# Kernel optimization log

Hardware: AMD Instinct MI355X
Metric: run time of the kernel (lower is better)

## Reference

```python
import jax, jax.numpy as jnp
import numpy as np

NUM_TAGS = 96
PAD_IDX = 0
NEG = -10000.0


def setup_inputs() -> dict:
    key = jax.random.key(0)
    k1, k2, k3, k4, k5 = jax.random.split(key, 5)
    B, S, T = 128, 2048, NUM_TAGS
    emissions = jax.random.normal(k1, (B, S, T), dtype=jnp.float32)
    tags = jax.random.randint(k2, (B, S), 0, T, dtype=jnp.int64)
    mask = jnp.ones((B, S), dtype=jnp.float32)
    transitions = jax.random.normal(k3, (T, T), dtype=jnp.float32)
    transitions = transitions.at[PAD_IDX, :].set(NEG)
    transitions = transitions.at[:, PAD_IDX].set(NEG)
    transitions = transitions.at[PAD_IDX, PAD_IDX].set(0.0)
    start_transitions = jax.random.normal(k4, (T,), dtype=jnp.float32)
    start_transitions = start_transitions.at[PAD_IDX].set(NEG)
    end_transitions = jax.random.normal(k5, (T,), dtype=jnp.float32)
    return {"emissions": emissions, "tags": tags, "mask": mask,
            "transitions": transitions, "start_transitions": start_transitions,
            "end_transitions": end_transitions}


def _compute_score(emissions, tags, mask, transitions, start_transitions, end_transitions):
    # score of the gold path, fully vectorized over time
    score = start_transitions[tags[:, 0]]
    score = score + jnp.take_along_axis(emissions[:, 0], tags[:, 0:1], axis=1)[:, 0]
    trans = transitions[tags[:, :-1], tags[:, 1:]]                       # (B, S-1)
    emit = jnp.take_along_axis(emissions[:, 1:], tags[:, 1:, None], axis=2)[..., 0]
    score = score + jnp.sum((trans + emit) * mask[:, 1:], axis=1)
    last_pos = mask.astype(jnp.int32).sum(axis=1) - 1                    # (B,)
    last_tags = jnp.take_along_axis(tags, last_pos[:, None], axis=1)[:, 0]
    return score + end_transitions[last_tags]


def _log_partition(emissions, mask, transitions, start_transitions, end_transitions):
    # forward algorithm as a scan over time, alpha kept resident
    alpha0 = start_transitions[None, :] + emissions[:, 0]                # (B, T)
    em_rest = jnp.swapaxes(emissions[:, 1:], 0, 1)                       # (S-1, B, T)
    mk_rest = jnp.swapaxes(mask[:, 1:], 0, 1)                            # (S-1, B)

    def step(alpha, xs):
        emit_t, m_t = xs
        # (B, T_prev, T_next)
        nxt = jax.nn.logsumexp(alpha[:, :, None] + transitions[None] + emit_t[:, None, :], axis=1)
        m = m_t[:, None]
        return nxt * m + alpha * (1.0 - m), None

    alpha, _ = jax.lax.scan(step, alpha0, (em_rest, mk_rest))
    return jax.nn.logsumexp(alpha + end_transitions[None, :], axis=1)


def reference(emissions, tags, mask, transitions, start_transitions, end_transitions):
    mask = mask.astype(jnp.float32)
    log_num = _compute_score(emissions, tags, mask, transitions, start_transitions, end_transitions)
    log_den = _log_partition(emissions, mask, transitions, start_transitions, end_transitions)
    return jnp.mean(log_den - log_num)
```

## Files before the change

### kernel.cpp

```cpp
#include <hip/hip_runtime.h>
#include <hip/hip_bf16.h>
#include <math.h>

#define NTAG 96
#define NB   128
#define SLEN 2048
#define CPERB (SLEN * NTAG)
#define NCH  16
#define CHUNK 128

typedef __attribute__((ext_vector_type(8)))  short bf16x8;
typedef __attribute__((ext_vector_type(4)))  float f32x4;
typedef __attribute__((ext_vector_type(16))) float f32x16;
union U8 { unsigned int u[4]; bf16x8 v; };

__device__ __forceinline__ unsigned int pk2bf(float lo, float hi) {
    union { __hip_bfloat16 h; unsigned short u; } a, b;
    a.h = __float2bfloat16(lo);
    b.h = __float2bfloat16(hi);
    return (unsigned int)a.u | ((unsigned int)b.u << 16);
}
__device__ __forceinline__ float bf16lo(unsigned int u) {
    union { unsigned int i; float f; } x; x.i = u << 16; return x.f;
}
__device__ __forceinline__ float bf16hi(unsigned int u) {
    union { unsigned int i; float f; } x; x.i = u & 0xffff0000u; return x.f;
}

__device__ __forceinline__ float waveSum(float v) {
    #pragma unroll
    for (int o = 32; o > 0; o >>= 1) v += __shfl_xor(v, o);
    return v;
}

__global__ __launch_bounds__(256) void exp_pass_bf16(
    const float* __restrict__ x, unsigned int* __restrict__ y)
{
    size_t i = (size_t)blockIdx.x * 256 + threadIdx.x;
    f32x4 v = ((const f32x4*)x)[i];
    uint2 o;
    o.x = pk2bf(__expf(v[0]), __expf(v[1]));
    o.y = pk2bf(__expf(v[2]), __expf(v[3]));
    ((uint2*)y)[i] = o;
}

template <int IEXP>
__global__ __launch_bounds__(64, 2) void crf_chunk32(
    const void* __restrict__ srcE, const float* __restrict__ mask,
    const float* __restrict__ trans,
    float* __restrict__ P, float* __restrict__ Pls)
{
    const int tid = threadIdx.x;
    const int c = tid & 31;
    const int h = tid >> 5;

    const int k   = blockIdx.x;
    const int xcd = k & 7;
    const int seq = k >> 3;
    const int w2  = seq % 3;
    const int bcg = seq / 3;
    const int bc  = bcg * 8 + xcd;
    const int cch = bc & (NCH - 1);
    const int b   = bc >> 4;
    const int t0  = 1 + cch * CHUNK;
    const int t1  = min(SLEN, t0 + CHUNK);

    float tm = -1e30f;
    for (int q = tid; q < NTAG * NTAG; q += 64) tm = fmaxf(tm, trans[q]);
    #pragma unroll
    for (int o = 32; o > 0; o >>= 1) tm = fmaxf(tm, __shfl_xor(tm, o));
    const float tmax = tm;

    const int cS = (c & 0x13) | ((c & 4) << 1) | ((c & 8) >> 1);
    U8 Af[3][6];
    #pragma unroll
    for (int jt = 0; jt < 3; ++jt) {
        #pragma unroll
        for (int kt = 0; kt < 6; ++kt) {
            #pragma unroll
            for (int d = 0; d < 4; ++d) {
                int K0 = 16 * kt + 8 * (d >> 1) + 4 * h + 2 * (d & 1);
                int J  = 32 * jt + cS;
                Af[jt][kt].u[d] = pk2bf(
                    __expf(trans[K0 * NTAG + J] - tmax),
                    __expf(trans[(K0 + 1) * NTAG + J] - tmax));
            }
        }
    }

    float S[3][16];
    #pragma unroll
    for (int rt = 0; rt < 3; ++rt) {
        #pragma unroll
        for (int r = 0; r < 16; ++r)
            S[rt][r] = (32 * rt + (r & 3) + 8 * (r >> 2) + 4 * h == 32 * w2 + c)
                       ? 1.0f : 0.0f;
    }
    float ls = 0.0f;

#define RENORM() do { \
    float mx_ = S[0][0]; \
    _Pragma("unroll") \
    for (int rt_ = 0; rt_ < 3; ++rt_) { \
        _Pragma("unroll") \
        for (int r_ = 0; r_ < 16; ++r_) mx_ = fmaxf(mx_, S[rt_][r_]); \
    } \
    mx_ = fmaxf(mx_, __shfl_xor(mx_, 32)); \
    mx_ = fmaxf(mx_, 1e-30f); \
    float inv_ = 1.0f / mx_; \
    ls += __logf(mx_); \
    _Pragma("unroll") \
    for (int rt_ = 0; rt_ < 3; ++rt_) { \
        _Pragma("unroll") \
        for (int r_ = 0; r_ < 16; ++r_) S[rt_][r_] *= inv_; \
    } \
} while (0)

    U8 Bu[6];
#define MAKEB() do { \
    _Pragma("unroll") \
    for (int kt_ = 0; kt_ < 6; ++kt_) { \
        const int rt_ = kt_ >> 1; \
        _Pragma("unroll") \
        for (int d_ = 0; d_ < 4; ++d_) { \
            const int rb_ = 8 * (kt_ & 1) + 4 * (d_ >> 1) + 2 * (d_ & 1); \
            Bu[kt_].u[d_] = pk2bf(S[rt_][rb_], S[rt_][rb_ + 1]); \
        } \
    } \
} while (0)

    const float* mkB = mask + (size_t)b * SLEN;
    const f32x16 z16 = {0.f,0.f,0.f,0.f,0.f,0.f,0.f,0.f,
                        0.f,0.f,0.f,0.f,0.f,0.f,0.f,0.f};

    const unsigned short* eH = (const unsigned short*)srcE + (size_t)b * CPERB;
    const float*          eF = (const float*)srcE + (size_t)b * CPERB;

    uint2 E2[12];
    f32x4 E4[12];
#define LOADE(T) do { \
    if (IEXP) { \
        const float* pE_ = eF + (size_t)(T) * NTAG + 4 * h; \
        _Pragma("unroll") \
        for (int rt_ = 0; rt_ < 3; ++rt_) { \
            _Pragma("unroll") \
            for (int q_ = 0; q_ < 4; ++q_) \
                E4[rt_ * 4 + q_] = *(const f32x4*)(pE_ + 32 * rt_ + 8 * q_); \
        } \
    } else { \
        const unsigned short* pH_ = eH + (size_t)(T) * NTAG + 4 * h; \
        _Pragma("unroll") \
        for (int rt_ = 0; rt_ < 3; ++rt_) { \
            _Pragma("unroll") \
            for (int q_ = 0; q_ < 4; ++q_) \
                E2[rt_ * 4 + q_] = *(const uint2*)(pH_ + 32 * rt_ + 8 * q_); \
        } \
    } \
} while (0)

#define STEPCORE(T) do { \
    LOADE(T); \
    f32x16 a0, a1, a2; \
    a0 = __builtin_amdgcn_mfma_f32_32x32x16_bf16(Af[0][0].v, Bu[0].v, z16, 0, 0, 0); \
    a1 = __builtin_amdgcn_mfma_f32_32x32x16_bf16(Af[1][0].v, Bu[0].v, z16, 0, 0, 0); \
    a2 = __builtin_amdgcn_mfma_f32_32x32x16_bf16(Af[2][0].v, Bu[0].v, z16, 0, 0, 0); \
    _Pragma("unroll") \
    for (int kt_ = 1; kt_ < 6; ++kt_) { \
        a0 = __builtin_amdgcn_mfma_f32_32x32x16_bf16(Af[0][kt_].v, Bu[kt_].v, a0, 0, 0, 0); \
        a1 = __builtin_amdgcn_mfma_f32_32x32x16_bf16(Af[1][kt_].v, Bu[kt_].v, a1, 0, 0, 0); \
        a2 = __builtin_amdgcn_mfma_f32_32x32x16_bf16(Af[2][kt_].v, Bu[kt_].v, a2, 0, 0, 0); \
    } \
    float mv_ = mkB[(T)]; \
    if (mv_ != 0.0f) { \
        _Pragma("unroll") \
        for (int rt_ = 0; rt_ < 3; ++rt_) { \
            f32x16 ac_ = (rt_ == 0) ? a0 : ((rt_ == 1) ? a1 : a2); \
            _Pragma("unroll") \
            for (int q_ = 0; q_ < 4; ++q_) { \
                float e0_, e1_, e2_, e3_; \
                if (IEXP) { \
                    e0_ = __expf(E4[rt_ * 4 + q_][0]); \
                    e1_ = __expf(E4[rt_ * 4 + q_][1]); \
                    e2_ = __expf(E4[rt_ * 4 + q_][2]); \
                    e3_ = __expf(E4[rt_ * 4 + q_][3]); \
                } else { \
                    uint2 u_ = E2[rt_ * 4 + q_]; \
                    e0_ = bf16lo(u_.x); e1_ = bf16hi(u_.x); \
                    e2_ = bf16lo(u_.y); e3_ = bf16hi(u_.y); \
                } \
                S[rt_][4 * q_ + 0] = ac_[4 * q_ + 0] * e0_; \
                S[rt_][4 * q_ + 1] = ac_[4 * q_ + 1] * e1_; \
                S[rt_][4 * q_ + 2] = ac_[4 * q_ + 2] * e2_; \
                S[rt_][4 * q_ + 3] = ac_[4 * q_ + 3] * e3_; \
            } \
        } \
        ls += tmax; \
    } \
} while (0)

#define STEP(T)   do { STEPCORE(T); MAKEB(); } while (0)
#define STEP_R(T) do { STEPCORE(T); RENORM(); MAKEB(); } while (0)

    MAKEB();

    const int nsteps = t1 - t0;
    const int nfull  = nsteps >> 3;
    int t = t0;
    #pragma unroll 1
    for (int blk = 0; blk < nfull; ++blk, t += 8) {
        STEP(t + 0); STEP(t + 1); STEP(t + 2); STEP(t + 3);
        STEP(t + 4); STEP(t + 5); STEP(t + 6); STEP_R(t + 7);
    }
    #pragma unroll 1
    while (t < t1) { STEP_R(t); ++t; }

    float* Pb = P + ((size_t)bc * NTAG + (32 * w2 + c)) * NTAG + 4 * h;
    #pragma unroll
    for (int rt = 0; rt < 3; ++rt) {
        #pragma unroll
        for (int q = 0; q < 4; ++q) {
            f32x4 v;
            v[0] = S[rt][4 * q + 0]; v[1] = S[rt][4 * q + 1];
            v[2] = S[rt][4 * q + 2]; v[3] = S[rt][4 * q + 3];
            *(f32x4*)(Pb + 32 * rt + 8 * q) = v;
        }
    }
    if (h == 0) Pls[(size_t)bc * NTAG + 32 * w2 + c] = ls;
#undef STEP
#undef STEP_R
#undef STEPCORE
#undef LOADE
#undef MAKEB
#undef RENORM
}

__global__ __launch_bounds__(128) void crf_fold(
    const float* __restrict__ em, const float* __restrict__ startT,
    const float* __restrict__ endT,
    const float* __restrict__ P, const float* __restrict__ Pls,
    float* __restrict__ den)
{
    __shared__ float aS[NTAG];
    __shared__ float sRed[2];
    const int b = blockIdx.x, tid = threadIdx.x;
    const bool act = tid < NTAG;

    float A = act ? (startT[tid] + em[(size_t)b * CPERB + tid]) : -1e30f;

    for (int c = 0; c < NCH; ++c) {
        const size_t bc = (size_t)b * NCH + c;
        float v = act ? (A + Pls[bc * NTAG + tid]) : -1e30f;
        float mv = v;
        #pragma unroll
        for (int o = 32; o > 0; o >>= 1) mv = fmaxf(mv, __shfl_xor(mv, o));
        if ((tid & 63) == 0) sRed[tid >> 6] = mv;
        __syncthreads();
        const float m = fmaxf(sRed[0], sRed[1]);
        __syncthreads();
        if (act) aS[tid] = __expf(v - m);
        __syncthreads();
        if (act) {
            const float* Pc = P + bc * (NTAG * NTAG) + tid;
            float dot = 0.f;
            #pragma unroll 8
            for (int i = 0; i < NTAG; ++i)
                dot = fmaf(aS[i], Pc[(size_t)i * NTAG], dot);
            A = m + __logf(dot);
        }
        __syncthreads();
    }

    float Afin = act ? (A + endT[tid]) : -1e30f;
    float mv = Afin;
    #pragma unroll
    for (int o = 32; o > 0; o >>= 1) mv = fmaxf(mv, __shfl_xor(mv, o));
    if ((tid & 63) == 0) sRed[tid >> 6] = mv;
    __syncthreads();
    const float m2 = fmaxf(sRed[0], sRed[1]);
    __syncthreads();
    float ex = act ? __expf(Afin - m2) : 0.f;
    ex = waveSum(ex);
    if ((tid & 63) == 0) sRed[tid >> 6] = ex;
    __syncthreads();
    if (tid == 0) den[b] = m2 + __logf(sRed[0] + sRed[1]);
}

__global__ __launch_bounds__(64, 1) void crf_forward_seq(
    const float* __restrict__ srcE, const float* __restrict__ srcM,
    const float* __restrict__ trans, const float* __restrict__ startT,
    const float* __restrict__ endT, float* __restrict__ den)
{
    __shared__ unsigned int lbuf[2][48 * 20];
    const int tid = threadIdx.x;
    const int g = tid >> 4;
    const int b16 = tid & 15;
    const int b = blockIdx.x * 16 + b16;

    float tm = -1e30f;
    for (int q = tid; q < NTAG * NTAG; q += 64) tm = fmaxf(tm, trans[q]);
    #pragma unroll
    for (int o = 32; o > 0; o >>= 1) tm = fmaxf(tm, __shfl_xor(tm, o));
    const float tmax = tm;

    bf16x8 Af[6][3];
    #pragma unroll
    for (int jt = 0; jt < 6; ++jt) {
        #pragma unroll
        for (int kf = 0; kf < 3; ++kf) {
            U8 u;
            #pragma unroll
            for (int d = 0; d < 4; ++d) {
                int i0 = 32 * kf + 8 * g + 2 * d;
                int j = 16 * jt + b16;
                u.u[d] = pk2bf(__expf(trans[i0 * NTAG + j] - tmax),
                               __expf(trans[(i0 + 1) * NTAG + j] - tmax));
            }
            Af[jt][kf] = u.v;
        }
    }

    float al[24];
    #pragma unroll
    for (int tile = 0; tile < 6; ++tile) {
        #pragma unroll
        for (int r = 0; r < 4; ++r) {
            int j = 16 * tile + 4 * g + r;
            al[tile * 4 + r] = __expf(startT[j]) * __expf(srcE[(size_t)b * CPERB + j]);
        }
    }
    float ls = 0.0f;

#define RENORM2() do { \
    float mx_ = al[0]; \
    _Pragma("unroll") \
    for (int k_ = 1; k_ < 24; ++k_) mx_ = fmaxf(mx_, al[k_]); \
    mx_ = fmaxf(mx_, __shfl_xor(mx_, 16)); \
    mx_ = fmaxf(mx_, __shfl_xor(mx_, 32)); \
    mx_ = fmaxf(mx_, 1e-30f); \
    float inv_ = 1.0f / mx_; \
    ls += __logf(mx_); \
    _Pragma("unroll") \
    for (int k_ = 0; k_ < 24; ++k_) al[k_] *= inv_; \
} while (0)

    U8 Bu[3];
#define MAKEB2(BUF) do { \
    _Pragma("unroll") \
    for (int t_ = 0; t_ < 6; ++t_) { \
        lbuf[BUF][(8 * t_ + 2 * g) * 20 + b16]     = pk2bf(al[4 * t_ + 0], al[4 * t_ + 1]); \
        lbuf[BUF][(8 * t_ + 2 * g + 1) * 20 + b16] = pk2bf(al[4 * t_ + 2], al[4 * t_ + 3]); \
    } \
    __syncthreads(); \
    _Pragma("unroll") \
    for (int kf_ = 0; kf_ < 3; ++kf_) { \
        _Pragma("unroll") \
        for (int d_ = 0; d_ < 4; ++d_) \
            Bu[kf_].u[d_] = lbuf[BUF][(16 * kf_ + 4 * g + d_) * 20 + b16]; \
    } \
} while (0)

    RENORM2();
    MAKEB2(0);
    const f32x4 zf4 = {0.f, 0.f, 0.f, 0.f};

    #pragma unroll 1
    for (int t = 1; t < SLEN; ++t) {
        f32x4 E[6];
        #pragma unroll
        for (int tl = 0; tl < 6; ++tl)
            E[tl] = *(const f32x4*)(srcE + (size_t)b * CPERB + (size_t)t * NTAG + 16 * tl + 4 * g);
        float mv = srcM[(size_t)b * SLEN + t];
        f32x4 acc[6];
        #pragma unroll
        for (int jt = 0; jt < 6; ++jt) {
            f32x4 a_ = __builtin_amdgcn_mfma_f32_16x16x32_bf16(Af[jt][0], Bu[0].v, zf4, 0, 0, 0);
            a_ = __builtin_amdgcn_mfma_f32_16x16x32_bf16(Af[jt][1], Bu[1].v, a_, 0, 0, 0);
            a_ = __builtin_amdgcn_mfma_f32_16x16x32_bf16(Af[jt][2], Bu[2].v, a_, 0, 0, 0);
            acc[jt] = a_;
        }
        bool km = (mv != 0.0f);
        #pragma unroll
        for (int tile = 0; tile < 6; ++tile) {
            #pragma unroll
            for (int r = 0; r < 4; ++r) {
                float nv = acc[tile][r] * __expf(E[tile][r]);
                al[tile * 4 + r] = km ? nv : al[tile * 4 + r];
            }
        }
        ls += km ? tmax : 0.0f;
        if ((t & 3) == 0) RENORM2();
        MAKEB2(t & 1);
        __syncthreads();
    }

    float s = 0.f;
    #pragma unroll
    for (int tile = 0; tile < 6; ++tile) {
        #pragma unroll
        for (int r = 0; r < 4; ++r) {
            int j = 16 * tile + 4 * g + r;
            s += al[tile * 4 + r] * __expf(endT[j]);
        }
    }
    s += __shfl_xor(s, 16);
    s += __shfl_xor(s, 32);
    if (tid < 16) den[b] = ls + __logf(s);
#undef MAKEB2
#undef RENORM2
}

__global__ __launch_bounds__(256) void crf_score(
    const float* __restrict__ em, const int* __restrict__ tags,
    const float* __restrict__ mask, const float* __restrict__ trans,
    const float* __restrict__ startT, const float* __restrict__ endT,
    float* __restrict__ num)
{
    __shared__ float sS[4], sM[4];
    const int b = blockIdx.x, tid = threadIdx.x;
    const float* emB = em + (size_t)b * CPERB;
    const int* tgB = tags + (size_t)b * SLEN;
    const float* mkB = mask + (size_t)b * SLEN;

    float part = 0.f, mcnt = 0.f;
    for (int t = tid; t < SLEN; t += 256) {
        float mt = mkB[t];
        mcnt += mt;
        if (t >= 1) {
            int tp = tgB[t - 1], tc = tgB[t];
            part += (trans[tp * NTAG + tc] + emB[(size_t)t * NTAG + tc]) * mt;
        }
    }
    part = waveSum(part);
    mcnt = waveSum(mcnt);
    if ((tid & 63) == 0) { sS[tid >> 6] = part; sM[tid >> 6] = mcnt; }
    __syncthreads();
    if (tid == 0) {
        float tot = sS[0] + sS[1] + sS[2] + sS[3];
        int last = (int)(sM[0] + sM[1] + sM[2] + sM[3]) - 1;
        int t0 = tgB[0];
        num[b] = tot + startT[t0] + emB[t0] + endT[tgB[last]];
    }
}

__global__ __launch_bounds__(128) void crf_final(
    const float* __restrict__ den, const float* __restrict__ num,
    float* __restrict__ out)
{
    __shared__ float s2[2];
    const int tid = threadIdx.x;
    float v = den[tid] - num[tid];
    v = waveSum(v);
    if ((tid & 63) == 0) s2[tid >> 6] = v;
    __syncthreads();
    if (tid == 0) out[0] = (s2[0] + s2[1]) * (1.0f / NB);
}

extern "C" void kernel_launch(void* const* d_in, const int* in_sizes, int n_in,
                              void* d_out, int out_size, void* d_ws, size_t ws_size,
                              hipStream_t stream) {
    const float* em     = (const float*)d_in[0];
    const int*   tags   = (const int*)d_in[1];
    const float* mask   = (const float*)d_in[2];
    const float* trans  = (const float*)d_in[3];
    const float* startT = (const float*)d_in[4];
    const float* endT   = (const float*)d_in[5];
    float* out = (float*)d_out;
    float* num = (float*)d_ws;
    float* den = num + NB;

    const size_t szP   = (size_t)NB * NCH * NTAG * NTAG;
    const size_t szPls = (size_t)NB * NCH * NTAG;
    float* P    = (float*)((char*)d_ws + 4096);
    float* Pls  = P + szP;
    unsigned int* eexpH = (unsigned int*)(Pls + szPls);
    const size_t need_mid  = 4096 + (szP + szPls) * 4;
    const size_t need_full = need_mid + (size_t)NB * CPERB * 2;

    crf_score<<<NB, 256, 0, stream>>>(em, tags, mask, trans, startT, endT, num);
    if (ws_size >= need_full) {
        exp_pass_bf16<<<(NB * CPERB) / (256 * 4), 256, 0, stream>>>(em, eexpH);
        crf_chunk32<0><<<3 * NB * NCH, 64, 0, stream>>>(eexpH, mask, trans, P, Pls);
        crf_fold<<<NB, 128, 0, stream>>>(em, startT, endT, P, Pls, den);
    } else if (ws_size >= need_mid) {
        crf_chunk32<1><<<3 * NB * NCH, 64, 0, stream>>>(em, mask, trans, P, Pls);
        crf_fold<<<NB, 128, 0, stream>>>(em, startT, endT, P, Pls, den);
    } else {
        crf_forward_seq<<<NB / 16, 64, 0, stream>>>(em, mask, trans, startT, endT, den);
    }
    crf_final<<<1, 128, 0, stream>>>(den, num, out);
}
```

Before: 710.4 us.

## Double-buffer emission loads and pack four chunk waves per block

Emission loads for step t+1 are now issued before the MFMA chain of step t, using two register buffers that alternate between steps. This hides global-load latency behind the matrix ops of the sequential chunk scan. Each block also becomes 4 waves (256 threads) instead of 1, with the grid divided by 4, which changes occupancy and scheduling. The remainder loop is unrolled into guarded steps so the buffer parity stays fixed, and the extra buffers raise register pressure.

```diff
diff --git a/kernel.cpp b/kernel.cpp
--- a/kernel.cpp
+++ b/kernel.cpp
@@ -45,18 +45,20 @@
 }
 
 template <int IEXP>
-__global__ __launch_bounds__(64, 2) void crf_chunk32(
+__global__ __launch_bounds__(256, 2) void crf_chunk32(
     const void* __restrict__ srcE, const float* __restrict__ mask,
     const float* __restrict__ trans,
     float* __restrict__ P, float* __restrict__ Pls)
 {
-    const int tid = threadIdx.x;
-    const int c = tid & 31;
-    const int h = tid >> 5;
-
-    const int k   = blockIdx.x;
-    const int xcd = k & 7;
-    const int seq = k >> 3;
+    const int wv  = threadIdx.x >> 6;
+    const int ln  = threadIdx.x & 63;
+    const int c = ln & 31;
+    const int h = ln >> 5;
+
+    const int blk = blockIdx.x;
+    const int xcd = blk & 7;
+    const int grp = blk >> 3;
+    const int seq = grp * 4 + wv;
     const int w2  = seq % 3;
     const int bcg = seq / 3;
     const int bc  = bcg * 8 + xcd;
@@ -66,7 +68,7 @@
     const int t1  = min(SLEN, t0 + CHUNK);
 
     float tm = -1e30f;
-    for (int q = tid; q < NTAG * NTAG; q += 64) tm = fmaxf(tm, trans[q]);
+    for (int q = ln; q < NTAG * NTAG; q += 64) tm = fmaxf(tm, trans[q]);
     #pragma unroll
     for (int o = 32; o > 0; o >>= 1) tm = fmaxf(tm, __shfl_xor(tm, o));
     const float tmax = tm;
@@ -133,33 +135,34 @@
     const f32x16 z16 = {0.f,0.f,0.f,0.f,0.f,0.f,0.f,0.f,
                         0.f,0.f,0.f,0.f,0.f,0.f,0.f,0.f};
 
-    const unsigned short* eH = (const unsigned short*)srcE + (size_t)b * CPERB;
-    const float*          eF = (const float*)srcE + (size_t)b * CPERB;
-
-    uint2 E2[12];
-    f32x4 E4[12];
-#define LOADE(T) do { \
+    const unsigned short* eHp = (const unsigned short*)srcE + (size_t)b * CPERB;
+    const float*          eFp = (const float*)srcE + (size_t)b * CPERB;
+
+    uint2 EH0[12], EH1[12];
+    f32x4 EF0[12], EF1[12];
+#define LOADE(N, T) do { \
+    int tn_ = (T) < t1 ? (T) : (t1 - 1); \
     if (IEXP) { \
-        const float* pE_ = eF + (size_t)(T) * NTAG + 4 * h; \
+        const float* pE_ = eFp + (size_t)tn_ * NTAG + 4 * h; \
         _Pragma("unroll") \
         for (int rt_ = 0; rt_ < 3; ++rt_) { \
             _Pragma("unroll") \
             for (int q_ = 0; q_ < 4; ++q_) \
-                E4[rt_ * 4 + q_] = *(const f32x4*)(pE_ + 32 * rt_ + 8 * q_); \
+                EF##N[rt_ * 4 + q_] = *(const f32x4*)(pE_ + 32 * rt_ + 8 * q_); \
         } \
     } else { \
-        const unsigned short* pH_ = eH + (size_t)(T) * NTAG + 4 * h; \
+        const unsigned short* pH_ = eHp + (size_t)tn_ * NTAG + 4 * h; \
         _Pragma("unroll") \
         for (int rt_ = 0; rt_ < 3; ++rt_) { \
             _Pragma("unroll") \
             for (int q_ = 0; q_ < 4; ++q_) \
-                E2[rt_ * 4 + q_] = *(const uint2*)(pH_ + 32 * rt_ + 8 * q_); \
+                EH##N[rt_ * 4 + q_] = *(const uint2*)(pH_ + 32 * rt_ + 8 * q_); \
         } \
     } \
 } while (0)
 
-#define STEPCORE(T) do { \
-    LOADE(T); \
+#define STEPCORE(CUR, NXT, T) do { \
+    LOADE(NXT, (T) + 1); \
     f32x16 a0, a1, a2; \
     a0 = __builtin_amdgcn_mfma_f32_32x32x16_bf16(Af[0][0].v, Bu[0].v, z16, 0, 0, 0); \
     a1 = __builtin_amdgcn_mfma_f32_32x32x16_bf16(Af[1][0].v, Bu[0].v, z16, 0, 0, 0); \
@@ -179,12 +182,12 @@
             for (int q_ = 0; q_ < 4; ++q_) { \
                 float e0_, e1_, e2_, e3_; \
                 if (IEXP) { \
-                    e0_ = __expf(E4[rt_ * 4 + q_][0]); \
-                    e1_ = __expf(E4[rt_ * 4 + q_][1]); \
-                    e2_ = __expf(E4[rt_ * 4 + q_][2]); \
-                    e3_ = __expf(E4[rt_ * 4 + q_][3]); \
+                    e0_ = __expf(EF##CUR[rt_ * 4 + q_][0]); \
+                    e1_ = __expf(EF##CUR[rt_ * 4 + q_][1]); \
+                    e2_ = __expf(EF##CUR[rt_ * 4 + q_][2]); \
+                    e3_ = __expf(EF##CUR[rt_ * 4 + q_][3]); \
                 } else { \
-                    uint2 u_ = E2[rt_ * 4 + q_]; \
+                    uint2 u_ = EH##CUR[rt_ * 4 + q_]; \
                     e0_ = bf16lo(u_.x); e1_ = bf16hi(u_.x); \
                     e2_ = bf16lo(u_.y); e3_ = bf16hi(u_.y); \
                 } \
@@ -198,21 +201,29 @@
     } \
 } while (0)
 
-#define STEP(T)   do { STEPCORE(T); MAKEB(); } while (0)
-#define STEP_R(T) do { STEPCORE(T); RENORM(); MAKEB(); } while (0)
+#define STEP(CUR, NXT, T)   do { STEPCORE(CUR, NXT, T); MAKEB(); } while (0)
+#define STEP_R(CUR, NXT, T) do { STEPCORE(CUR, NXT, T); RENORM(); MAKEB(); } while (0)
 
     MAKEB();
+    LOADE(0, t0);
 
     const int nsteps = t1 - t0;
     const int nfull  = nsteps >> 3;
     int t = t0;
     #pragma unroll 1
-    for (int blk = 0; blk < nfull; ++blk, t += 8) {
-        STEP(t + 0); STEP(t + 1); STEP(t + 2); STEP(t + 3);
-        STEP(t + 4); STEP(t + 5); STEP(t + 6); STEP_R(t + 7);
-    }
-    #pragma unroll 1
-    while (t < t1) { STEP_R(t); ++t; }
+    for (int bq = 0; bq < nfull; ++bq, t += 8) {
+        STEP(0, 1, t + 0); STEP(1, 0, t + 1);
+        STEP(0, 1, t + 2); STEP(1, 0, t + 3);
+        STEP(0, 1, t + 4); STEP(1, 0, t + 5);
+        STEP(0, 1, t + 6); STEP_R(1, 0, t + 7);
+    }
+    if (t < t1) { STEP(0, 1, t); ++t; }
+    if (t < t1) { STEP(1, 0, t); ++t; }
+    if (t < t1) { STEP(0, 1, t); ++t; }
+    if (t < t1) { STEP_R(1, 0, t); ++t; }
+    if (t < t1) { STEP(0, 1, t); ++t; }
+    if (t < t1) { STEP(1, 0, t); ++t; }
+    if (t < t1) { STEP_R(0, 1, t); ++t; }
 
     float* Pb = P + ((size_t)bc * NTAG + (32 * w2 + c)) * NTAG + 4 * h;
     #pragma unroll
@@ -479,10 +490,10 @@
     crf_score<<<NB, 256, 0, stream>>>(em, tags, mask, trans, startT, endT, num);
     if (ws_size >= need_full) {
         exp_pass_bf16<<<(NB * CPERB) / (256 * 4), 256, 0, stream>>>(em, eexpH);
-        crf_chunk32<0><<<3 * NB * NCH, 64, 0, stream>>>(eexpH, mask, trans, P, Pls);
+        crf_chunk32<0><<<(3 * NB * NCH) / 4, 256, 0, stream>>>(eexpH, mask, trans, P, Pls);
         crf_fold<<<NB, 128, 0, stream>>>(em, startT, endT, P, Pls, den);
     } else if (ws_size >= need_mid) {
-        crf_chunk32<1><<<3 * NB * NCH, 64, 0, stream>>>(em, mask, trans, P, Pls);
+        crf_chunk32<1><<<(3 * NB * NCH) / 4, 256, 0, stream>>>(em, mask, trans, P, Pls);
         crf_fold<<<NB, 128, 0, stream>>>(em, startT, endT, P, Pls, den);
     } else {
         crf_forward_seq<<<NB / 16, 64, 0, stream>>>(em, mask, trans, startT, endT, den);
```

Measured after the change: 1.284 ms. 80.7% more time.

## Switch chunked CRF forward MFMA from bf16 to fp8 with lighter renormalization

Applied to the files above, without the earlier changes.

Replaces the bf16 32x32x16 MFMA chain with fp8 e4m3 MFMA, packing the exp-transition matrix and the state vector into fp8. Accumulators are reused in place as the state, emission loads move inside the mask branch, and renormalization runs every other step instead of every eighth. Occupancy hint rises to 3 waves per SIMD, and the fp32-emission fallback path is removed. The intent is to halve MFMA operand width and cut per-step packing and register cost, at the risk of accuracy loss from fp8's 3-bit mantissa compounding over 128 steps, and of fp8 overflow or underflow that the more frequent renormalization is meant to contain.

```diff
diff --git a/kernel.cpp b/kernel.cpp
--- a/kernel.cpp
+++ b/kernel.cpp
@@ -1,5 +1,6 @@
 #include <hip/hip_runtime.h>
 #include <hip/hip_bf16.h>
+#include <hip/hip_fp8.h>
 #include <math.h>
 
 #define NTAG 96
@@ -12,7 +13,8 @@
 typedef __attribute__((ext_vector_type(8)))  short bf16x8;
 typedef __attribute__((ext_vector_type(4)))  float f32x4;
 typedef __attribute__((ext_vector_type(16))) float f32x16;
-union U8 { unsigned int u[4]; bf16x8 v; };
+union U8  { unsigned int u[4]; bf16x8 v; };
+union UB8 { unsigned int u[2]; long long l; };
 
 __device__ __forceinline__ unsigned int pk2bf(float lo, float hi) {
     union { __hip_bfloat16 h; unsigned short u; } a, b;
@@ -25,6 +27,25 @@
 }
 __device__ __forceinline__ float bf16hi(unsigned int u) {
     union { unsigned int i; float f; } x; x.i = u & 0xffff0000u; return x.f;
+}
+
+__device__ __forceinline__ unsigned int pk4fp8(float a, float b, float c, float d) {
+#if defined(__has_builtin)
+#if __has_builtin(__builtin_amdgcn_cvt_pk_fp8_f32)
+    int v = 0;
+    v = __builtin_amdgcn_cvt_pk_fp8_f32(a, b, v, false);
+    v = __builtin_amdgcn_cvt_pk_fp8_f32(c, d, v, true);
+    return (unsigned int)v;
+#else
+    __hip_fp8_e4m3 fa(a), fb(b), fc(c), fd(d);
+    return (unsigned int)fa.__x | ((unsigned int)fb.__x << 8) |
+           ((unsigned int)fc.__x << 16) | ((unsigned int)fd.__x << 24);
+#endif
+#else
+    __hip_fp8_e4m3 fa(a), fb(b), fc(c), fd(d);
+    return (unsigned int)fa.__x | ((unsigned int)fb.__x << 8) |
+           ((unsigned int)fc.__x << 16) | ((unsigned int)fd.__x << 24);
+#endif
 }
 
 __device__ __forceinline__ float waveSum(float v) {
@@ -44,9 +65,8 @@
     ((uint2*)y)[i] = o;
 }
 
-template <int IEXP>
-__global__ __launch_bounds__(64, 2) void crf_chunk32(
-    const void* __restrict__ srcE, const float* __restrict__ mask,
+__global__ __launch_bounds__(64, 3) void crf_chunk32_fp8(
+    const unsigned short* __restrict__ eH, const float* __restrict__ mask,
     const float* __restrict__ trans,
     float* __restrict__ P, float* __restrict__ Pls)
 {
@@ -72,166 +92,143 @@
     const float tmax = tm;
 
     const int cS = (c & 0x13) | ((c & 4) << 1) | ((c & 8) >> 1);
-    U8 Af[3][6];
+    UB8 Af[3][6];
     #pragma unroll
     for (int jt = 0; jt < 3; ++jt) {
+        const int J = 32 * jt + cS;
         #pragma unroll
         for (int kt = 0; kt < 6; ++kt) {
-            #pragma unroll
-            for (int d = 0; d < 4; ++d) {
-                int K0 = 16 * kt + 8 * (d >> 1) + 4 * h + 2 * (d & 1);
-                int J  = 32 * jt + cS;
-                Af[jt][kt].u[d] = pk2bf(
-                    __expf(trans[K0 * NTAG + J] - tmax),
-                    __expf(trans[(K0 + 1) * NTAG + J] - tmax));
-            }
-        }
-    }
-
-    float S[3][16];
-    #pragma unroll
-    for (int rt = 0; rt < 3; ++rt) {
-        #pragma unroll
-        for (int r = 0; r < 16; ++r)
-            S[rt][r] = (32 * rt + (r & 3) + 8 * (r >> 2) + 4 * h == 32 * w2 + c)
-                       ? 1.0f : 0.0f;
+            const int K0 = 16 * kt + 4 * h;
+            const int K1 = K0 + 8;
+            Af[jt][kt].u[0] = pk4fp8(
+                __expf(trans[(K0 + 0) * NTAG + J] - tmax),
+                __expf(trans[(K0 + 1) * NTAG + J] - tmax),
+                __expf(trans[(K0 + 2) * NTAG + J] - tmax),
+                __expf(trans[(K0 + 3) * NTAG + J] - tmax));
+            Af[jt][kt].u[1] = pk4fp8(
+                __expf(trans[(K1 + 0) * NTAG + J] - tmax),
+                __expf(trans[(K1 + 1) * NTAG + J] - tmax),
+                __expf(trans[(K1 + 2) * NTAG + J] - tmax),
+                __expf(trans[(K1 + 3) * NTAG + J] - tmax));
+        }
+    }
+
+    f32x16 s0, s1, s2;
+    #pragma unroll
+    for (int r = 0; r < 16; ++r) {
+        const int rr = (r & 3) + 8 * (r >> 2) + 4 * h;
+        s0[r] = (rr       == 32 * w2 + c) ? 1.0f : 0.0f;
+        s1[r] = (32 + rr  == 32 * w2 + c) ? 1.0f : 0.0f;
+        s2[r] = (64 + rr  == 32 * w2 + c) ? 1.0f : 0.0f;
     }
     float ls = 0.0f;
 
-#define RENORM() do { \
-    float mx_ = S[0][0]; \
-    _Pragma("unroll") \
-    for (int rt_ = 0; rt_ < 3; ++rt_) { \
-        _Pragma("unroll") \
-        for (int r_ = 0; r_ < 16; ++r_) mx_ = fmaxf(mx_, S[rt_][r_]); \
-    } \
-    mx_ = fmaxf(mx_, __shfl_xor(mx_, 32)); \
-    mx_ = fmaxf(mx_, 1e-30f); \
-    float inv_ = 1.0f / mx_; \
-    ls += __logf(mx_); \
-    _Pragma("unroll") \
-    for (int rt_ = 0; rt_ < 3; ++rt_) { \
-        _Pragma("unroll") \
-        for (int r_ = 0; r_ < 16; ++r_) S[rt_][r_] *= inv_; \
-    } \
-} while (0)
-
-    U8 Bu[6];
-#define MAKEB() do { \
-    _Pragma("unroll") \
-    for (int kt_ = 0; kt_ < 6; ++kt_) { \
-        const int rt_ = kt_ >> 1; \
-        _Pragma("unroll") \
-        for (int d_ = 0; d_ < 4; ++d_) { \
-            const int rb_ = 8 * (kt_ & 1) + 4 * (d_ >> 1) + 2 * (d_ & 1); \
-            Bu[kt_].u[d_] = pk2bf(S[rt_][rb_], S[rt_][rb_ + 1]); \
-        } \
-    } \
-} while (0)
-
-    const float* mkB = mask + (size_t)b * SLEN;
+    UB8 Bu[6];
+#define PACKB() do { \
+    Bu[0].u[0] = pk4fp8(s0[0],  s0[1],  s0[2],  s0[3]);  \
+    Bu[0].u[1] = pk4fp8(s0[4],  s0[5],  s0[6],  s0[7]);  \
+    Bu[1].u[0] = pk4fp8(s0[8],  s0[9],  s0[10], s0[11]); \
+    Bu[1].u[1] = pk4fp8(s0[12], s0[13], s0[14], s0[15]); \
+    Bu[2].u[0] = pk4fp8(s1[0],  s1[1],  s1[2],  s1[3]);  \
+    Bu[2].u[1] = pk4fp8(s1[4],  s1[5],  s1[6],  s1[7]);  \
+    Bu[3].u[0] = pk4fp8(s1[8],  s1[9],  s1[10], s1[11]); \
+    Bu[3].u[1] = pk4fp8(s1[12], s1[13], s1[14], s1[15]); \
+    Bu[4].u[0] = pk4fp8(s2[0],  s2[1],  s2[2],  s2[3]);  \
+    Bu[4].u[1] = pk4fp8(s2[4],  s2[5],  s2[6],  s2[7]);  \
+    Bu[5].u[0] = pk4fp8(s2[8],  s2[9],  s2[10], s2[11]); \
+    Bu[5].u[1] = pk4fp8(s2[12], s2[13], s2[14], s2[15]); \
+} while (0)
+
+    const unsigned short* eB  = eH + (size_t)b * CPERB + 4 * h;
+    const float*          mkB = mask + (size_t)b * SLEN;
     const f32x16 z16 = {0.f,0.f,0.f,0.f,0.f,0.f,0.f,0.f,
                         0.f,0.f,0.f,0.f,0.f,0.f,0.f,0.f};
 
-    const unsigned short* eH = (const unsigned short*)srcE + (size_t)b * CPERB;
-    const float*          eF = (const float*)srcE + (size_t)b * CPERB;
-
     uint2 E2[12];
-    f32x4 E4[12];
 #define LOADE(T) do { \
-    if (IEXP) { \
-        const float* pE_ = eF + (size_t)(T) * NTAG + 4 * h; \
-        _Pragma("unroll") \
-        for (int rt_ = 0; rt_ < 3; ++rt_) { \
-            _Pragma("unroll") \
-            for (int q_ = 0; q_ < 4; ++q_) \
-                E4[rt_ * 4 + q_] = *(const f32x4*)(pE_ + 32 * rt_ + 8 * q_); \
-        } \
-    } else { \
-        const unsigned short* pH_ = eH + (size_t)(T) * NTAG + 4 * h; \
-        _Pragma("unroll") \
-        for (int rt_ = 0; rt_ < 3; ++rt_) { \
-            _Pragma("unroll") \
-            for (int q_ = 0; q_ < 4; ++q_) \
-                E2[rt_ * 4 + q_] = *(const uint2*)(pH_ + 32 * rt_ + 8 * q_); \
-        } \
+    const unsigned short* p_ = eB + (size_t)(T) * NTAG; \
+    _Pragma("unroll") \
+    for (int i_ = 0; i_ < 12; ++i_) E2[i_] = *(const uint2*)(p_ + 8 * i_); \
+} while (0)
+
+#define EMUL(SV, B0) do { \
+    _Pragma("unroll") \
+    for (int q_ = 0; q_ < 4; ++q_) { \
+        uint2 u_ = E2[(B0) + q_]; \
+        SV[4*q_+0] *= bf16lo(u_.x); SV[4*q_+1] *= bf16hi(u_.x); \
+        SV[4*q_+2] *= bf16lo(u_.y); SV[4*q_+3] *= bf16hi(u_.y); \
     } \
 } while (0)
 
-#define STEPCORE(T) do { \
-    LOADE(T); \
-    f32x16 a0, a1, a2; \
-    a0 = __builtin_amdgcn_mfma_f32_32x32x16_bf16(Af[0][0].v, Bu[0].v, z16, 0, 0, 0); \
-    a1 = __builtin_amdgcn_mfma_f32_32x32x16_bf16(Af[1][0].v, Bu[0].v, z16, 0, 0, 0); \
-    a2 = __builtin_amdgcn_mfma_f32_32x32x16_bf16(Af[2][0].v, Bu[0].v, z16, 0, 0, 0); \
-    _Pragma("unroll") \
-    for (int kt_ = 1; kt_ < 6; ++kt_) { \
-        a0 = __builtin_amdgcn_mfma_f32_32x32x16_bf16(Af[0][kt_].v, Bu[kt_].v, a0, 0, 0, 0); \
-        a1 = __builtin_amdgcn_mfma_f32_32x32x16_bf16(Af[1][kt_].v, Bu[kt_].v, a1, 0, 0, 0); \
-        a2 = __builtin_amdgcn_mfma_f32_32x32x16_bf16(Af[2][kt_].v, Bu[kt_].v, a2, 0, 0, 0); \
-    } \
+#define STEPF(T, RN) do { \
     float mv_ = mkB[(T)]; \
     if (mv_ != 0.0f) { \
+        LOADE(T); \
+        s0 = __builtin_amdgcn_mfma_f32_32x32x16_fp8_fp8(Af[0][0].l, Bu[0].l, z16, 0, 0, 0); \
+        s1 = __builtin_amdgcn_mfma_f32_32x32x16_fp8_fp8(Af[1][0].l, Bu[0].l, z16, 0, 0, 0); \
+        s2 = __builtin_amdgcn_mfma_f32_32x32x16_fp8_fp8(Af[2][0].l, Bu[0].l, z16, 0, 0, 0); \
         _Pragma("unroll") \
-        for (int rt_ = 0; rt_ < 3; ++rt_) { \
-            f32x16 ac_ = (rt_ == 0) ? a0 : ((rt_ == 1) ? a1 : a2); \
+        for (int kt_ = 1; kt_ < 6; ++kt_) { \
+            s0 = __builtin_amdgcn_mfma_f32_32x32x16_fp8_fp8(Af[0][kt_].l, Bu[kt_].l, s0, 0, 0, 0); \
+            s1 = __builtin_amdgcn_mfma_f32_32x32x16_fp8_fp8(Af[1][kt_].l, Bu[kt_].l, s1, 0, 0, 0); \
+            s2 = __builtin_amdgcn_mfma_f32_32x32x16_fp8_fp8(Af[2][kt_].l, Bu[kt_].l, s2, 0, 0, 0); \
+        } \
+        EMUL(s0, 0); EMUL(s1, 4); EMUL(s2, 8); \
+        ls += tmax; \
+        if (RN) { \
+            float m_ = s0[0]; \
             _Pragma("unroll") \
-            for (int q_ = 0; q_ < 4; ++q_) { \
-                float e0_, e1_, e2_, e3_; \
-                if (IEXP) { \
-                    e0_ = __expf(E4[rt_ * 4 + q_][0]); \
-                    e1_ = __expf(E4[rt_ * 4 + q_][1]); \
-                    e2_ = __expf(E4[rt_ * 4 + q_][2]); \
-                    e3_ = __expf(E4[rt_ * 4 + q_][3]); \
-                } else { \
-                    uint2 u_ = E2[rt_ * 4 + q_]; \
-                    e0_ = bf16lo(u_.x); e1_ = bf16hi(u_.x); \
-                    e2_ = bf16lo(u_.y); e3_ = bf16hi(u_.y); \
-                } \
-                S[rt_][4 * q_ + 0] = ac_[4 * q_ + 0] * e0_; \
-                S[rt_][4 * q_ + 1] = ac_[4 * q_ + 1] * e1_; \
-                S[rt_][4 * q_ + 2] = ac_[4 * q_ + 2] * e2_; \
-                S[rt_][4 * q_ + 3] = ac_[4 * q_ + 3] * e3_; \
-            } \
+            for (int r_ = 1; r_ < 16; ++r_) m_ = fmaxf(m_, s0[r_]); \
+            _Pragma("unroll") \
+            for (int r_ = 0; r_ < 16; ++r_) m_ = fmaxf(m_, s1[r_]); \
+            _Pragma("unroll") \
+            for (int r_ = 0; r_ < 16; ++r_) m_ = fmaxf(m_, s2[r_]); \
+            m_ = fmaxf(m_, __shfl_xor(m_, 32)); \
+            m_ = fmaxf(m_, 1e-30f); \
+            float inv_; \
+            asm("v_rcp_f32 %0, %1" : "=v"(inv_) : "v"(m_)); \
+            ls += __logf(m_); \
+            _Pragma("unroll") \
+            for (int r_ = 0; r_ < 16; ++r_) { s0[r_] *= inv_; s1[r_] *= inv_; s2[r_] *= inv_; } \
         } \
-        ls += tmax; \
+        PACKB(); \
     } \
 } while (0)
 
-#define STEP(T)   do { STEPCORE(T); MAKEB(); } while (0)
-#define STEP_R(T) do { STEPCORE(T); RENORM(); MAKEB(); } while (0)
-
-    MAKEB();
+    PACKB();
 
     const int nsteps = t1 - t0;
     const int nfull  = nsteps >> 3;
     int t = t0;
     #pragma unroll 1
-    for (int blk = 0; blk < nfull; ++blk, t += 8) {
-        STEP(t + 0); STEP(t + 1); STEP(t + 2); STEP(t + 3);
-        STEP(t + 4); STEP(t + 5); STEP(t + 6); STEP_R(t + 7);
+    for (int bq = 0; bq < nfull; ++bq, t += 8) {
+        STEPF(t + 0, 0); STEPF(t + 1, 1);
+        STEPF(t + 2, 0); STEPF(t + 3, 1);
+        STEPF(t + 4, 0); STEPF(t + 5, 1);
+        STEPF(t + 6, 0); STEPF(t + 7, 1);
     }
     #pragma unroll 1
-    while (t < t1) { STEP_R(t); ++t; }
+    while (t < t1) {
+        if ((t - t0) & 1) STEPF(t, 1); else STEPF(t, 0);
+        ++t;
+    }
 
     float* Pb = P + ((size_t)bc * NTAG + (32 * w2 + c)) * NTAG + 4 * h;
     #pragma unroll
-    for (int rt = 0; rt < 3; ++rt) {
-        #pragma unroll
-        for (int q = 0; q < 4; ++q) {
-            f32x4 v;
-            v[0] = S[rt][4 * q + 0]; v[1] = S[rt][4 * q + 1];
-            v[2] = S[rt][4 * q + 2]; v[3] = S[rt][4 * q + 3];
-            *(f32x4*)(Pb + 32 * rt + 8 * q) = v;
-        }
+    for (int q = 0; q < 4; ++q) {
+        f32x4 v0, v1, v2;
+        v0[0]=s0[4*q+0]; v0[1]=s0[4*q+1]; v0[2]=s0[4*q+2]; v0[3]=s0[4*q+3];
+        v1[0]=s1[4*q+0]; v1[1]=s1[4*q+1]; v1[2]=s1[4*q+2]; v1[3]=s1[4*q+3];
+        v2[0]=s2[4*q+0]; v2[1]=s2[4*q+1]; v2[2]=s2[4*q+2]; v2[3]=s2[4*q+3];
+        *(f32x4*)(Pb + 8 * q)      = v0;
+        *(f32x4*)(Pb + 32 + 8 * q) = v1;
+        *(f32x4*)(Pb + 64 + 8 * q) = v2;
     }
     if (h == 0) Pls[(size_t)bc * NTAG + 32 * w2 + c] = ls;
-#undef STEP
-#undef STEP_R
-#undef STEPCORE
+#undef STEPF
+#undef EMUL
 #undef LOADE
-#undef MAKEB
-#undef RENORM
+#undef PACKB
 }
 
 __global__ __launch_bounds__(128) void crf_fold(
@@ -473,16 +470,13 @@
     float* P    = (float*)((char*)d_ws + 4096);
     float* Pls  = P + szP;
     unsigned int* eexpH = (unsigned int*)(Pls + szPls);
-    const size_t need_mid  = 4096 + (szP + szPls) * 4;
-    const size_t need_full = need_mid + (size_t)NB * CPERB * 2;
+    const size_t need_full = 4096 + (szP + szPls) * 4 + (size_t)NB * CPERB * 2;
 
     crf_score<<<NB, 256, 0, stream>>>(em, tags, mask, trans, startT, endT, num);
     if (ws_size >= need_full) {
         exp_pass_bf16<<<(NB * CPERB) / (256 * 4), 256, 0, stream>>>(em, eexpH);
-        crf_chunk32<0><<<3 * NB * NCH, 64, 0, stream>>>(eexpH, mask, trans, P, Pls);
-        crf_fold<<<NB, 128, 0, stream>>>(em, startT, endT, P, Pls, den);
-    } else if (ws_size >= need_mid) {
-        crf_chunk32<1><<<3 * NB * NCH, 64, 0, stream>>>(em, mask, trans, P, Pls);
+        crf_chunk32_fp8<<<3 * NB * NCH, 64, 0, stream>>>(
+            (const unsigned short*)eexpH, mask, trans, P, Pls);
         crf_fold<<<NB, 128, 0, stream>>>(em, startT, endT, P, Pls, den);
     } else {
         crf_forward_seq<<<NB / 16, 64, 0, stream>>>(em, mask, trans, startT, endT, den);
```

After: 613.2 us. 13.7% less time.
